# Performance work log

Measured on AMD Instinct MI355X. Metric: run time of the kernel, lower is better.

Reference implementation:

```python
import jax, jax.numpy as jnp
import numpy as np

TIME_STEP = 0.1
ITER_NUM = 10
ALPHA = 0.01


def _conv3x3(x, w, b):
    # x: [N,C,H,W], w: [O,C,3,3], b: [O]; SAME padding, stride 1
    y = jax.lax.conv_general_dilated(
        x, w, window_strides=(1, 1), padding=((1, 1), (1, 1)),
        dimension_numbers=("NCHW", "OIHW", "NCHW"))
    return y + b[None, :, None, None]


def _nonlin(x, alpha=ALPHA):
    y = jnp.minimum(x, 1.0 + alpha * (x - 1.0))
    return jnp.maximum(y, -1.0 + alpha * (y + 1.0))


def setup_inputs() -> dict:
    key = jax.random.key(0)
    ks = jax.random.split(key, 8)
    N, Ci, Co, H, W = 16, 64, 64, 128, 128
    fan_in = Ci * 9
    bound = 1.0 / np.sqrt(fan_in)
    x = jax.random.normal(ks[0], (N, Ci, H, W), dtype=jnp.float32)
    rescale_w = jax.random.uniform(ks[1], (Co, Ci, 3, 3), minval=-bound, maxval=bound, dtype=jnp.float32)
    rescale_b = jax.random.uniform(ks[2], (Co,), minval=-bound, maxval=bound, dtype=jnp.float32)
    bound_a = 1.0 / np.sqrt(Co * 9)
    A_w = jax.random.uniform(ks[3], (Co, Co, 3, 3), minval=-bound_a, maxval=bound_a, dtype=jnp.float32)
    A_b = jax.random.uniform(ks[4], (Co,), minval=-bound_a, maxval=bound_a, dtype=jnp.float32)
    B_w = jax.random.uniform(ks[5], (Co, Ci, 3, 3), minval=-bound, maxval=bound, dtype=jnp.float32)
    B_b = jax.random.uniform(ks[6], (Co,), minval=-bound, maxval=bound, dtype=jnp.float32)
    Z = jax.random.normal(ks[7], (Co,), dtype=jnp.float32)
    return {"x": x, "rescale_w": rescale_w, "rescale_b": rescale_b,
            "A_w": A_w, "A_b": A_b, "B_w": B_w, "B_b": B_b, "Z": Z}


def reference(x, rescale_w, rescale_b, A_w, A_b, B_w, B_b, Z):
    input_coupling = _conv3x3(x, B_w, B_b) + Z[None, :, None, None]
    state = _conv3x3(x, rescale_w, rescale_b)

    def body(i, s):
        coupling = _conv3x3(_nonlin(s), A_w, A_b) + input_coupling
        return s + TIME_STEP * (-s + coupling)

    state = jax.lax.fori_loop(0, ITER_NUM, body, state)
    return _nonlin(state)
```

## Files before the change

kernel.cpp:

```cpp
#include <hip/hip_runtime.h>


typedef short  bf16x8 __attribute__((ext_vector_type(8)));
typedef float  f32x4  __attribute__((ext_vector_type(4)));

#define HH 128
#define WW 128
#define NCH 64
#define GROWS 8
#define NSLOT 10
#define XS 32
#define NC 34
#define ROWB 128
#define SLOTB (NC * ROWB)
#define ACTB (NSLOT * SLOTB)
#define WSETB 73728

__device__ __align__(16) unsigned char g_fw[3 * WSETB];

__device__ __forceinline__ float nonlin(float x) {
    const float A = 0.01f;
    float y = fminf(x, fmaf(A, x, 1.0f - A));
    return fmaxf(y, fmaf(A, y, -(1.0f - A)));
}
__device__ __forceinline__ unsigned int f2bf(float f) {
    unsigned int u = __float_as_uint(f);
    u += 0x7fffu + ((u >> 16) & 1u);
    return u >> 16;
}

__global__ __launch_bounds__(256)
void prep_w(const float* __restrict__ rw, const float* __restrict__ bw,
            const float* __restrict__ aw) {
    const float* w = blockIdx.x == 0 ? rw : (blockIdx.x == 1 ? bw : aw);
    unsigned char* o = g_fw + blockIdx.x * WSETB;
    int chunk = blockIdx.y * 256 + threadIdx.x;
    int cb  = chunk / 1152;
    int rem = chunk - cb * 1152;
    int kb  = rem >> 6;
    int ln  = rem & 63;
    int cout = cb * 16 + (ln & 15);
    int g    = ln >> 4;
    unsigned int h[8];
    #pragma unroll
    for (int j = 0; j < 8; ++j) {
        int k = kb * 32 + g * 8 + j;
        int tap = k >> 6;
        int cin = k & 63;
        h[j] = f2bf(w[(cout * 64 + cin) * 9 + tap]);
    }
    uint4 v;
    v.x = h[0] | (h[1] << 16);
    v.y = h[2] | (h[3] << 16);
    v.z = h[4] | (h[5] << 16);
    v.w = h[6] | (h[7] << 16);
    *(uint4*)(o + chunk * 16) = v;
}

__device__ __forceinline__ void conv_tile(const char* actl, const unsigned char* fw,
                                          int lane, int wv, f32x4 (&acc)[4][4]) {
    const int l15 = lane & 15;
    const int g4  = lane >> 4;
    #pragma unroll
    for (int kb = 0; kb < 18; ++kb) {
        const int tap  = kb >> 1;
        const int dy   = tap / 3;
        const int dx   = tap - dy * 3;
        const int cinB = (kb & 1) * 64 + g4 * 16;
        bf16x8 af[4];
        #pragma unroll
        for (int cb = 0; cb < 4; ++cb)
            af[cb] = *(const bf16x8*)(fw + ((cb * 18 + kb) * 64 + lane) * 16);
        bf16x8 bfr[4];
        #pragma unroll
        for (int i = 0; i < 4; ++i) {
            int row = wv * 2 + (i >> 1) + dy;
            int c   = (i & 1) * 16 + l15 + dx;
            bfr[i] = *(const bf16x8*)(actl + row * SLOTB + c * ROWB
                                      + (cinB ^ ((c & 7) << 4)));
        }
        #pragma unroll
        for (int cb = 0; cb < 4; ++cb)
            #pragma unroll
            for (int i = 0; i < 4; ++i)
                acc[cb][i] = __builtin_amdgcn_mfma_f32_16x16x32_bf16(
                    af[cb], bfr[i], acc[cb][i], 0, 0, 0);
    }
}

template<int MODE>
__global__ __launch_bounds__(256, 3)
void cenn(const float* __restrict__ src,
          const float* __restrict__ rb, const float* __restrict__ bb,
          const float* __restrict__ zz, const float* __restrict__ ab,
          const float* __restrict__ icp,
          float* __restrict__ dst, float* __restrict__ dst2)
{
    __shared__ __align__(16) char actl[ACTB];
    const int tid  = threadIdx.x;
    const int lane = tid & 63;
    const int wv   = tid >> 6;
    const int l15  = lane & 15;
    const int g4   = lane >> 4;

    int lin = (blockIdx.z * 16 + blockIdx.y) * 4 + blockIdx.x;
    lin = (lin & 7) * 128 + (lin >> 3);
    const int x0 = (lin & 3) * XS;
    const int y0 = ((lin >> 2) & 15) * GROWS;
    const int n  = lin >> 6;

    if constexpr (MODE == 0) {
        for (int idx = tid; idx < NSLOT * NC * 8; idx += 256) {
            int r   = idx / (NC * 8);
            int rem = idx - r * (NC * 8);
            int cb8 = rem / NC;
            int c   = rem - cb8 * NC;
            int y   = y0 + r - 1;
            int x   = x0 + c - 1;
            uint4 v = {0u, 0u, 0u, 0u};
            if ((unsigned)y < (unsigned)HH && (unsigned)x < (unsigned)WW) {
                const float* p = src + ((size_t)(n * NCH + cb8 * 8) * HH + y) * WW + x;
                unsigned int h[8];
                #pragma unroll
                for (int j = 0; j < 8; ++j)
                    h[j] = f2bf(p[(size_t)j * HH * WW]);
                v.x = h[0] | (h[1] << 16);
                v.y = h[2] | (h[3] << 16);
                v.z = h[4] | (h[5] << 16);
                v.w = h[6] | (h[7] << 16);
            }
            *(uint4*)(actl + r * SLOTB + c * ROWB + ((cb8 * 16) ^ ((c & 7) << 4))) = v;
        }
    } else {
        for (int idx = tid; idx < NSLOT * NC * 16; idx += 256) {
            int r   = idx / (NC * 16);
            int rem = idx - r * (NC * 16);
            int c   = rem >> 4;
            int q   = rem & 15;
            int y   = y0 + r - 1;
            int x   = x0 + c - 1;
            uint2 w2 = {0u, 0u};
            if ((unsigned)y < (unsigned)HH && (unsigned)x < (unsigned)WW) {
                f32x4 v = *(const f32x4*)(src + ((((size_t)n * HH + y) * WW + x) << 6) + q * 4);
                w2.x = f2bf(nonlin(v[0])) | (f2bf(nonlin(v[1])) << 16);
                w2.y = f2bf(nonlin(v[2])) | (f2bf(nonlin(v[3])) << 16);
            }
            *(uint2*)(actl + r * SLOTB + c * ROWB + ((q * 8) ^ ((c & 7) << 4))) = w2;
        }
    }
    __syncthreads();

    f32x4 acc[4][4];
    #pragma unroll
    for (int a = 0; a < 4; ++a)
        #pragma unroll
        for (int b = 0; b < 4; ++b)
            acc[a][b] = (f32x4){0.f, 0.f, 0.f, 0.f};

    conv_tile(actl, g_fw + (MODE == 0 ? 0 : 2 * WSETB), lane, wv, acc);

    if constexpr (MODE == 0) {
        #pragma unroll
        for (int cb = 0; cb < 4; ++cb)
            #pragma unroll
            for (int i = 0; i < 4; ++i) {
                int y  = y0 + wv * 2 + (i >> 1);
                int x  = x0 + (i & 1) * 16 + l15;
                int c0 = cb * 16 + g4 * 4;
                size_t base = ((((size_t)n * HH + y) * WW + x) << 6) + c0;
                f32x4 o;
                #pragma unroll
                for (int r = 0; r < 4; ++r) o[r] = acc[cb][i][r] + rb[c0 + r];
                *(f32x4*)(dst + base) = o;
            }
        #pragma unroll
        for (int a = 0; a < 4; ++a)
            #pragma unroll
            for (int b = 0; b < 4; ++b)
                acc[a][b] = (f32x4){0.f, 0.f, 0.f, 0.f};
        conv_tile(actl, g_fw + WSETB, lane, wv, acc);
        #pragma unroll
        for (int cb = 0; cb < 4; ++cb)
            #pragma unroll
            for (int i = 0; i < 4; ++i) {
                int y  = y0 + wv * 2 + (i >> 1);
                int x  = x0 + (i & 1) * 16 + l15;
                int c0 = cb * 16 + g4 * 4;
                size_t base = ((((size_t)n * HH + y) * WW + x) << 6) + c0;
                f32x4 o;
                #pragma unroll
                for (int r = 0; r < 4; ++r)
                    o[r] = 0.1f * (acc[cb][i][r] + bb[c0 + r] + zz[c0 + r] + ab[c0 + r]);
                *(f32x4*)(dst2 + base) = o;
            }
    } else {
        #pragma unroll
        for (int rs = 0; rs < 2; ++rs) {
            __syncthreads();
            #pragma unroll
            for (int cb = 0; cb < 4; ++cb)
                #pragma unroll
                for (int fr = 0; fr < 2; ++fr) {
                    int i  = rs * 2 + fr;
                    int x  = fr * 16 + l15;
                    int cs = (cb * 16 + g4 * 4) ^ ((x & 7) << 2);
                    *(f32x4*)(actl + (((wv * 32 + x) << 6) + cs) * 4) = acc[cb][i];
                }
            __syncthreads();
            #pragma unroll
            for (int ps = 0; ps < 8; ++ps) {
                int t2   = ps * 256 + tid;
                int q    = t2 & 15;
                int px   = t2 >> 4;
                int x    = px & 31;
                int lrow = px >> 5;
                int cs   = (q * 4) ^ ((x & 7) << 2);
                f32x4 cv = *(const f32x4*)(actl + (((lrow * 32 + x) << 6) + cs) * 4);
                int y  = y0 + lrow * 2 + rs;
                int gx = x0 + x;
                size_t base = ((((size_t)n * HH + y) * WW + gx) << 6) + q * 4;
                f32x4 s = *(const f32x4*)(src + base);
                f32x4 p = *(const f32x4*)(icp + base);
                f32x4 o;
                #pragma unroll
                for (int r = 0; r < 4; ++r)
                    o[r] = 0.1f * cv[r] + 0.9f * s[r] + p[r];
                if constexpr (MODE == 1) {
                    *(f32x4*)(dst + base) = o;
                } else {
                    #pragma unroll
                    for (int r = 0; r < 4; ++r) o[r] = nonlin(o[r]);
                    *(f32x4*)(actl + (((lrow * 32 + x) << 6) + cs) * 4) = o;
                }
            }
            if constexpr (MODE == 2) {
                __syncthreads();
                #pragma unroll
                for (int ps = 0; ps < 8; ++ps) {
                    int xl   = tid & 15;
                    int xf   = (tid >> 4) & 1;
                    int qh   = tid >> 5;
                    int q    = (ps & 1) * 8 + qh;
                    int lrow = ps >> 1;
                    int x    = xf * 16 + xl;
                    int cs   = (q * 4) ^ ((x & 7) << 2);
                    f32x4 v  = *(const f32x4*)(actl + (((lrow * 32 + x) << 6) + cs) * 4);
                    int y  = y0 + lrow * 2 + rs;
                    int gx = x0 + x;
                    #pragma unroll
                    for (int j = 0; j < 4; ++j)
                        dst[((size_t)(n * NCH + q * 4 + j) * HH + y) * WW + gx] = v[j];
                }
            }
        }
    }
}

extern "C" void kernel_launch(void* const* d_in, const int* in_sizes, int n_in,
                              void* d_out, int out_size, void* d_ws, size_t ws_size,
                              hipStream_t stream) {
    const float* x  = (const float*)d_in[0];
    const float* rw = (const float*)d_in[1];
    const float* rb = (const float*)d_in[2];
    const float* aw = (const float*)d_in[3];
    const float* ab = (const float*)d_in[4];
    const float* bw = (const float*)d_in[5];
    const float* bb = (const float*)d_in[6];
    const float* z  = (const float*)d_in[7];
    float* out = (float*)d_out;

    const size_t P = (size_t)16 * NCH * HH * WW;
    float* icp = (float*)d_ws;
    float* s1  = icp + P;

    dim3 blk(256, 1, 1), grd(4, 16, 16);

    prep_w<<<dim3(3, 18, 1), blk, 0, stream>>>(rw, bw, aw);
    cenn<0><<<grd, blk, 0, stream>>>(x, rb, bb, z, ab, nullptr, out, icp);

    for (int i = 0; i < 10; ++i) {
        const float* s = (i & 1) ? s1 : out;
        float*       d = (i & 1) ? out : s1;
        if (i == 9)
            cenn<2><<<grd, blk, 0, stream>>>(s, nullptr, nullptr, nullptr, nullptr, icp, out, nullptr);
        else
            cenn<1><<<grd, blk, 0, stream>>>(s, nullptr, nullptr, nullptr, nullptr, icp, d, nullptr);
    }
}
```

Before: 619.9 us.

## Store input coupling in bf16 and fuse init convolutions into one pass

The precomputed input-coupling tensor is now stored as bf16 instead of fp32, which halves that read in each of the ten iteration kernels. The init kernel runs both convolutions in one interleaved MFMA loop sharing the activation fragments, using two accumulator sets and lowering the occupancy hint to 2. Init outputs are now written through an LDS transpose for coalesced stores. The cost is extra rounding error in the coupling term and higher register pressure in the init kernel.

```diff
diff --git a/kernel.cpp b/kernel.cpp
--- a/kernel.cpp
+++ b/kernel.cpp
@@ -88,13 +88,50 @@
     }
 }
 
-template<int MODE>
-__global__ __launch_bounds__(256, 3)
-void cenn(const float* __restrict__ src,
-          const float* __restrict__ rb, const float* __restrict__ bb,
-          const float* __restrict__ zz, const float* __restrict__ ab,
-          const float* __restrict__ icp,
-          float* __restrict__ dst, float* __restrict__ dst2)
+__device__ __forceinline__ void conv_tile2(const char* actl,
+                                           const unsigned char* fw0,
+                                           const unsigned char* fw1,
+                                           int lane, int wv,
+                                           f32x4 (&acc0)[4][4], f32x4 (&acc1)[4][4]) {
+    const int l15 = lane & 15;
+    const int g4  = lane >> 4;
+    #pragma unroll
+    for (int kb = 0; kb < 18; ++kb) {
+        const int tap  = kb >> 1;
+        const int dy   = tap / 3;
+        const int dx   = tap - dy * 3;
+        const int cinB = (kb & 1) * 64 + g4 * 16;
+        bf16x8 af0[4], af1[4];
+        #pragma unroll
+        for (int cb = 0; cb < 4; ++cb) {
+            af0[cb] = *(const bf16x8*)(fw0 + ((cb * 18 + kb) * 64 + lane) * 16);
+            af1[cb] = *(const bf16x8*)(fw1 + ((cb * 18 + kb) * 64 + lane) * 16);
+        }
+        bf16x8 bfr[4];
+        #pragma unroll
+        for (int i = 0; i < 4; ++i) {
+            int row = wv * 2 + (i >> 1) + dy;
+            int c   = (i & 1) * 16 + l15 + dx;
+            bfr[i] = *(const bf16x8*)(actl + row * SLOTB + c * ROWB
+                                      + (cinB ^ ((c & 7) << 4)));
+        }
+        #pragma unroll
+        for (int cb = 0; cb < 4; ++cb)
+            #pragma unroll
+            for (int i = 0; i < 4; ++i) {
+                acc0[cb][i] = __builtin_amdgcn_mfma_f32_16x16x32_bf16(
+                    af0[cb], bfr[i], acc0[cb][i], 0, 0, 0);
+                acc1[cb][i] = __builtin_amdgcn_mfma_f32_16x16x32_bf16(
+                    af1[cb], bfr[i], acc1[cb][i], 0, 0, 0);
+            }
+    }
+}
+
+__global__ __launch_bounds__(256, 2)
+void cenn_init(const float* __restrict__ src,
+               const float* __restrict__ rb, const float* __restrict__ bb,
+               const float* __restrict__ zz, const float* __restrict__ ab,
+               float* __restrict__ dst, unsigned short* __restrict__ icp)
 {
     __shared__ __align__(16) char actl[ACTB];
     const int tid  = threadIdx.x;
@@ -109,44 +146,143 @@
     const int y0 = ((lin >> 2) & 15) * GROWS;
     const int n  = lin >> 6;
 
-    if constexpr (MODE == 0) {
-        for (int idx = tid; idx < NSLOT * NC * 8; idx += 256) {
-            int r   = idx / (NC * 8);
-            int rem = idx - r * (NC * 8);
-            int cb8 = rem / NC;
-            int c   = rem - cb8 * NC;
-            int y   = y0 + r - 1;
-            int x   = x0 + c - 1;
-            uint4 v = {0u, 0u, 0u, 0u};
-            if ((unsigned)y < (unsigned)HH && (unsigned)x < (unsigned)WW) {
-                const float* p = src + ((size_t)(n * NCH + cb8 * 8) * HH + y) * WW + x;
-                unsigned int h[8];
-                #pragma unroll
-                for (int j = 0; j < 8; ++j)
-                    h[j] = f2bf(p[(size_t)j * HH * WW]);
-                v.x = h[0] | (h[1] << 16);
-                v.y = h[2] | (h[3] << 16);
-                v.z = h[4] | (h[5] << 16);
-                v.w = h[6] | (h[7] << 16);
-            }
-            *(uint4*)(actl + r * SLOTB + c * ROWB + ((cb8 * 16) ^ ((c & 7) << 4))) = v;
-        }
-    } else {
-        for (int idx = tid; idx < NSLOT * NC * 16; idx += 256) {
-            int r   = idx / (NC * 16);
-            int rem = idx - r * (NC * 16);
-            int c   = rem >> 4;
-            int q   = rem & 15;
-            int y   = y0 + r - 1;
-            int x   = x0 + c - 1;
-            uint2 w2 = {0u, 0u};
-            if ((unsigned)y < (unsigned)HH && (unsigned)x < (unsigned)WW) {
-                f32x4 v = *(const f32x4*)(src + ((((size_t)n * HH + y) * WW + x) << 6) + q * 4);
-                w2.x = f2bf(nonlin(v[0])) | (f2bf(nonlin(v[1])) << 16);
-                w2.y = f2bf(nonlin(v[2])) | (f2bf(nonlin(v[3])) << 16);
-            }
-            *(uint2*)(actl + r * SLOTB + c * ROWB + ((q * 8) ^ ((c & 7) << 4))) = w2;
-        }
+    for (int idx = tid; idx < NSLOT * NC * 8; idx += 256) {
+        int r   = idx / (NC * 8);
+        int rem = idx - r * (NC * 8);
+        int cb8 = rem / NC;
+        int c   = rem - cb8 * NC;
+        int y   = y0 + r - 1;
+        int x   = x0 + c - 1;
+        uint4 v = {0u, 0u, 0u, 0u};
+        if ((unsigned)y < (unsigned)HH && (unsigned)x < (unsigned)WW) {
+            const float* p = src + ((size_t)(n * NCH + cb8 * 8) * HH + y) * WW + x;
+            unsigned int h[8];
+            #pragma unroll
+            for (int j = 0; j < 8; ++j)
+                h[j] = f2bf(p[(size_t)j * HH * WW]);
+            v.x = h[0] | (h[1] << 16);
+            v.y = h[2] | (h[3] << 16);
+            v.z = h[4] | (h[5] << 16);
+            v.w = h[6] | (h[7] << 16);
+        }
+        *(uint4*)(actl + r * SLOTB + c * ROWB + ((cb8 * 16) ^ ((c & 7) << 4))) = v;
+    }
+    __syncthreads();
+
+    f32x4 acc0[4][4], acc1[4][4];
+    #pragma unroll
+    for (int a = 0; a < 4; ++a)
+        #pragma unroll
+        for (int b = 0; b < 4; ++b) {
+            acc0[a][b] = (f32x4){0.f, 0.f, 0.f, 0.f};
+            acc1[a][b] = (f32x4){0.f, 0.f, 0.f, 0.f};
+        }
+    conv_tile2(actl, g_fw, g_fw + WSETB, lane, wv, acc0, acc1);
+
+    const int q = tid & 15;
+    f32x4 brb = *(const f32x4*)(rb + q * 4);
+    f32x4 bic;
+    {
+        f32x4 b1 = *(const f32x4*)(bb + q * 4);
+        f32x4 b2 = *(const f32x4*)(zz + q * 4);
+        f32x4 b3 = *(const f32x4*)(ab + q * 4);
+        #pragma unroll
+        for (int r = 0; r < 4; ++r) bic[r] = 0.1f * (b1[r] + b2[r] + b3[r]);
+    }
+
+    #pragma unroll
+    for (int rs = 0; rs < 2; ++rs) {
+        __syncthreads();
+        #pragma unroll
+        for (int cb = 0; cb < 4; ++cb)
+            #pragma unroll
+            for (int fr = 0; fr < 2; ++fr) {
+                int x  = fr * 16 + l15;
+                int cs = (cb * 16 + g4 * 4) ^ ((x & 7) << 2);
+                *(f32x4*)(actl + (((wv * 32 + x) << 6) + cs) * 4) = acc0[cb][rs * 2 + fr];
+            }
+        __syncthreads();
+        #pragma unroll
+        for (int ps = 0; ps < 8; ++ps) {
+            int t2   = ps * 256 + tid;
+            int px   = t2 >> 4;
+            int x    = px & 31;
+            int lrow = px >> 5;
+            int cs   = (q * 4) ^ ((x & 7) << 2);
+            f32x4 cv = *(const f32x4*)(actl + (((lrow * 32 + x) << 6) + cs) * 4);
+            int y  = y0 + lrow * 2 + rs;
+            int gx = x0 + x;
+            size_t base = ((((size_t)n * HH + y) * WW + gx) << 6) + q * 4;
+            f32x4 o;
+            #pragma unroll
+            for (int r = 0; r < 4; ++r) o[r] = cv[r] + brb[r];
+            *(f32x4*)(dst + base) = o;
+        }
+        __syncthreads();
+        #pragma unroll
+        for (int cb = 0; cb < 4; ++cb)
+            #pragma unroll
+            for (int fr = 0; fr < 2; ++fr) {
+                int x  = fr * 16 + l15;
+                int cs = (cb * 16 + g4 * 4) ^ ((x & 7) << 2);
+                *(f32x4*)(actl + (((wv * 32 + x) << 6) + cs) * 4) = acc1[cb][rs * 2 + fr];
+            }
+        __syncthreads();
+        #pragma unroll
+        for (int ps = 0; ps < 8; ++ps) {
+            int t2   = ps * 256 + tid;
+            int px   = t2 >> 4;
+            int x    = px & 31;
+            int lrow = px >> 5;
+            int cs   = (q * 4) ^ ((x & 7) << 2);
+            f32x4 cv = *(const f32x4*)(actl + (((lrow * 32 + x) << 6) + cs) * 4);
+            int y  = y0 + lrow * 2 + rs;
+            int gx = x0 + x;
+            size_t base = ((((size_t)n * HH + y) * WW + gx) << 6) + q * 4;
+            f32x4 o;
+            #pragma unroll
+            for (int r = 0; r < 4; ++r) o[r] = 0.1f * cv[r] + bic[r];
+            uint2 w2;
+            w2.x = f2bf(o[0]) | (f2bf(o[1]) << 16);
+            w2.y = f2bf(o[2]) | (f2bf(o[3]) << 16);
+            *(uint2*)(icp + base) = w2;
+        }
+    }
+}
+
+template<int FINAL>
+__global__ __launch_bounds__(256, 3)
+void cenn_iter(const float* __restrict__ src,
+               const unsigned short* __restrict__ icp,
+               float* __restrict__ dst)
+{
+    __shared__ __align__(16) char actl[ACTB];
+    const int tid  = threadIdx.x;
+    const int lane = tid & 63;
+    const int wv   = tid >> 6;
+    const int l15  = lane & 15;
+    const int g4   = lane >> 4;
+
+    int lin = (blockIdx.z * 16 + blockIdx.y) * 4 + blockIdx.x;
+    lin = (lin & 7) * 128 + (lin >> 3);
+    const int x0 = (lin & 3) * XS;
+    const int y0 = ((lin >> 2) & 15) * GROWS;
+    const int n  = lin >> 6;
+
+    for (int idx = tid; idx < NSLOT * NC * 16; idx += 256) {
+        int r   = idx / (NC * 16);
+        int rem = idx - r * (NC * 16);
+        int c   = rem >> 4;
+        int qq  = rem & 15;
+        int y   = y0 + r - 1;
+        int x   = x0 + c - 1;
+        uint2 w2 = {0u, 0u};
+        if ((unsigned)y < (unsigned)HH && (unsigned)x < (unsigned)WW) {
+            f32x4 v = *(const f32x4*)(src + ((((size_t)n * HH + y) * WW + x) << 6) + qq * 4);
+            w2.x = f2bf(nonlin(v[0])) | (f2bf(nonlin(v[1])) << 16);
+            w2.y = f2bf(nonlin(v[2])) | (f2bf(nonlin(v[3])) << 16);
+        }
+        *(uint2*)(actl + r * SLOTB + c * ROWB + ((qq * 8) ^ ((c & 7) << 4))) = w2;
     }
     __syncthreads();
 
@@ -157,100 +293,68 @@
         for (int b = 0; b < 4; ++b)
             acc[a][b] = (f32x4){0.f, 0.f, 0.f, 0.f};
 
-    conv_tile(actl, g_fw + (MODE == 0 ? 0 : 2 * WSETB), lane, wv, acc);
-
-    if constexpr (MODE == 0) {
-        #pragma unroll
-        for (int cb = 0; cb < 4; ++cb)
-            #pragma unroll
-            for (int i = 0; i < 4; ++i) {
-                int y  = y0 + wv * 2 + (i >> 1);
-                int x  = x0 + (i & 1) * 16 + l15;
-                int c0 = cb * 16 + g4 * 4;
-                size_t base = ((((size_t)n * HH + y) * WW + x) << 6) + c0;
-                f32x4 o;
+    conv_tile(actl, g_fw + 2 * WSETB, lane, wv, acc);
+
+    const int q = tid & 15;
+    #pragma unroll
+    for (int rs = 0; rs < 2; ++rs) {
+        __syncthreads();
+        #pragma unroll
+        for (int cb = 0; cb < 4; ++cb)
+            #pragma unroll
+            for (int fr = 0; fr < 2; ++fr) {
+                int x  = fr * 16 + l15;
+                int cs = (cb * 16 + g4 * 4) ^ ((x & 7) << 2);
+                *(f32x4*)(actl + (((wv * 32 + x) << 6) + cs) * 4) = acc[cb][rs * 2 + fr];
+            }
+        __syncthreads();
+        #pragma unroll
+        for (int ps = 0; ps < 8; ++ps) {
+            int t2   = ps * 256 + tid;
+            int px   = t2 >> 4;
+            int x    = px & 31;
+            int lrow = px >> 5;
+            int cs   = (q * 4) ^ ((x & 7) << 2);
+            f32x4 cv = *(const f32x4*)(actl + (((lrow * 32 + x) << 6) + cs) * 4);
+            int y  = y0 + lrow * 2 + rs;
+            int gx = x0 + x;
+            size_t base = ((((size_t)n * HH + y) * WW + gx) << 6) + q * 4;
+            f32x4 s = *(const f32x4*)(src + base);
+            uint2 pw = *(const uint2*)(icp + base);
+            f32x4 p;
+            p[0] = __uint_as_float(pw.x << 16);
+            p[1] = __uint_as_float(pw.x & 0xffff0000u);
+            p[2] = __uint_as_float(pw.y << 16);
+            p[3] = __uint_as_float(pw.y & 0xffff0000u);
+            f32x4 o;
+            #pragma unroll
+            for (int r = 0; r < 4; ++r)
+                o[r] = 0.1f * cv[r] + 0.9f * s[r] + p[r];
+            if constexpr (FINAL == 0) {
+                *(f32x4*)(dst + base) = o;
+            } else {
                 #pragma unroll
-                for (int r = 0; r < 4; ++r) o[r] = acc[cb][i][r] + rb[c0 + r];
-                *(f32x4*)(dst + base) = o;
-            }
-        #pragma unroll
-        for (int a = 0; a < 4; ++a)
-            #pragma unroll
-            for (int b = 0; b < 4; ++b)
-                acc[a][b] = (f32x4){0.f, 0.f, 0.f, 0.f};
-        conv_tile(actl, g_fw + WSETB, lane, wv, acc);
-        #pragma unroll
-        for (int cb = 0; cb < 4; ++cb)
-            #pragma unroll
-            for (int i = 0; i < 4; ++i) {
-                int y  = y0 + wv * 2 + (i >> 1);
-                int x  = x0 + (i & 1) * 16 + l15;
-                int c0 = cb * 16 + g4 * 4;
-                size_t base = ((((size_t)n * HH + y) * WW + x) << 6) + c0;
-                f32x4 o;
-                #pragma unroll
-                for (int r = 0; r < 4; ++r)
-                    o[r] = 0.1f * (acc[cb][i][r] + bb[c0 + r] + zz[c0 + r] + ab[c0 + r]);
-                *(f32x4*)(dst2 + base) = o;
-            }
-    } else {
-        #pragma unroll
-        for (int rs = 0; rs < 2; ++rs) {
+                for (int r = 0; r < 4; ++r) o[r] = nonlin(o[r]);
+                *(f32x4*)(actl + (((lrow * 32 + x) << 6) + cs) * 4) = o;
+            }
+        }
+        if constexpr (FINAL == 1) {
             __syncthreads();
             #pragma unroll
-            for (int cb = 0; cb < 4; ++cb)
-                #pragma unroll
-                for (int fr = 0; fr < 2; ++fr) {
-                    int i  = rs * 2 + fr;
-                    int x  = fr * 16 + l15;
-                    int cs = (cb * 16 + g4 * 4) ^ ((x & 7) << 2);
-                    *(f32x4*)(actl + (((wv * 32 + x) << 6) + cs) * 4) = acc[cb][i];
-                }
-            __syncthreads();
-            #pragma unroll
             for (int ps = 0; ps < 8; ++ps) {
-                int t2   = ps * 256 + tid;
-                int q    = t2 & 15;
-                int px   = t2 >> 4;
-                int x    = px & 31;
-                int lrow = px >> 5;
-                int cs   = (q * 4) ^ ((x & 7) << 2);
-                f32x4 cv = *(const f32x4*)(actl + (((lrow * 32 + x) << 6) + cs) * 4);
+                int xl   = tid & 15;
+                int xf   = (tid >> 4) & 1;
+                int qh   = tid >> 5;
+                int qc   = (ps & 1) * 8 + qh;
+                int lrow = ps >> 1;
+                int x    = xf * 16 + xl;
+                int cs   = (qc * 4) ^ ((x & 7) << 2);
+                f32x4 v  = *(const f32x4*)(actl + (((lrow * 32 + x) << 6) + cs) * 4);
                 int y  = y0 + lrow * 2 + rs;
                 int gx = x0 + x;
-                size_t base = ((((size_t)n * HH + y) * WW + gx) << 6) + q * 4;
-                f32x4 s = *(const f32x4*)(src + base);
-                f32x4 p = *(const f32x4*)(icp + base);
-                f32x4 o;
                 #pragma unroll
-                for (int r = 0; r < 4; ++r)
-                    o[r] = 0.1f * cv[r] + 0.9f * s[r] + p[r];
-                if constexpr (MODE == 1) {
-                    *(f32x4*)(dst + base) = o;
-                } else {
-                    #pragma unroll
-                    for (int r = 0; r < 4; ++r) o[r] = nonlin(o[r]);
-                    *(f32x4*)(actl + (((lrow * 32 + x) << 6) + cs) * 4) = o;
-                }
-            }
-            if constexpr (MODE == 2) {
-                __syncthreads();
-                #pragma unroll
-                for (int ps = 0; ps < 8; ++ps) {
-                    int xl   = tid & 15;
-                    int xf   = (tid >> 4) & 1;
-                    int qh   = tid >> 5;
-                    int q    = (ps & 1) * 8 + qh;
-                    int lrow = ps >> 1;
-                    int x    = xf * 16 + xl;
-                    int cs   = (q * 4) ^ ((x & 7) << 2);
-                    f32x4 v  = *(const f32x4*)(actl + (((lrow * 32 + x) << 6) + cs) * 4);
-                    int y  = y0 + lrow * 2 + rs;
-                    int gx = x0 + x;
-                    #pragma unroll
-                    for (int j = 0; j < 4; ++j)
-                        dst[((size_t)(n * NCH + q * 4 + j) * HH + y) * WW + gx] = v[j];
-                }
+                for (int j = 0; j < 4; ++j)
+                    dst[((size_t)(n * NCH + qc * 4 + j) * HH + y) * WW + gx] = v[j];
             }
         }
     }
@@ -270,20 +374,20 @@
     float* out = (float*)d_out;
 
     const size_t P = (size_t)16 * NCH * HH * WW;
-    float* icp = (float*)d_ws;
-    float* s1  = icp + P;
+    unsigned short* icp = (unsigned short*)d_ws;
+    float* s1 = (float*)((char*)d_ws + 2 * P);
 
     dim3 blk(256, 1, 1), grd(4, 16, 16);
 
     prep_w<<<dim3(3, 18, 1), blk, 0, stream>>>(rw, bw, aw);
-    cenn<0><<<grd, blk, 0, stream>>>(x, rb, bb, z, ab, nullptr, out, icp);
+    cenn_init<<<grd, blk, 0, stream>>>(x, rb, bb, z, ab, out, icp);
 
     for (int i = 0; i < 10; ++i) {
         const float* s = (i & 1) ? s1 : out;
         float*       d = (i & 1) ? out : s1;
         if (i == 9)
-            cenn<2><<<grd, blk, 0, stream>>>(s, nullptr, nullptr, nullptr, nullptr, icp, out, nullptr);
+            cenn_iter<1><<<grd, blk, 0, stream>>>(s, icp, out);
         else
-            cenn<1><<<grd, blk, 0, stream>>>(s, nullptr, nullptr, nullptr, nullptr, icp, d, nullptr);
-    }
-}
+            cenn_iter<0><<<grd, blk, 0, stream>>>(s, icp, d);
+    }
+}
```

Result: no change. 621.3 us (+0.2%).

## Store input coupling in bf16 and reuse interior state loads in registers

Applied to the files above, without the earlier changes.

The precomputed input-coupling term is now stored as bf16 instead of fp32, which halves its read traffic in each of the ten iteration kernels. The iteration kernel also loads the halo cells separately from the interior. Interior state values are read once, converted to bf16 activations in shared memory, and the first row-half is kept in registers for the state update instead of being re-read from global memory. The cost is lower precision in the coupling term, which is added to the state every iteration.

```diff
diff --git a/kernel.cpp b/kernel.cpp
--- a/kernel.cpp
+++ b/kernel.cpp
@@ -88,13 +88,11 @@
     }
 }
 
-template<int MODE>
 __global__ __launch_bounds__(256, 3)
-void cenn(const float* __restrict__ src,
-          const float* __restrict__ rb, const float* __restrict__ bb,
-          const float* __restrict__ zz, const float* __restrict__ ab,
-          const float* __restrict__ icp,
-          float* __restrict__ dst, float* __restrict__ dst2)
+void cenn_init(const float* __restrict__ src,
+               const float* __restrict__ rb, const float* __restrict__ bb,
+               const float* __restrict__ zz, const float* __restrict__ ab,
+               float* __restrict__ dst, unsigned short* __restrict__ icp)
 {
     __shared__ __align__(16) char actl[ACTB];
     const int tid  = threadIdx.x;
@@ -109,36 +107,108 @@
     const int y0 = ((lin >> 2) & 15) * GROWS;
     const int n  = lin >> 6;
 
-    if constexpr (MODE == 0) {
-        for (int idx = tid; idx < NSLOT * NC * 8; idx += 256) {
-            int r   = idx / (NC * 8);
-            int rem = idx - r * (NC * 8);
-            int cb8 = rem / NC;
-            int c   = rem - cb8 * NC;
-            int y   = y0 + r - 1;
-            int x   = x0 + c - 1;
-            uint4 v = {0u, 0u, 0u, 0u};
-            if ((unsigned)y < (unsigned)HH && (unsigned)x < (unsigned)WW) {
-                const float* p = src + ((size_t)(n * NCH + cb8 * 8) * HH + y) * WW + x;
-                unsigned int h[8];
-                #pragma unroll
-                for (int j = 0; j < 8; ++j)
-                    h[j] = f2bf(p[(size_t)j * HH * WW]);
-                v.x = h[0] | (h[1] << 16);
-                v.y = h[2] | (h[3] << 16);
-                v.z = h[4] | (h[5] << 16);
-                v.w = h[6] | (h[7] << 16);
-            }
-            *(uint4*)(actl + r * SLOTB + c * ROWB + ((cb8 * 16) ^ ((c & 7) << 4))) = v;
-        }
-    } else {
-        for (int idx = tid; idx < NSLOT * NC * 16; idx += 256) {
-            int r   = idx / (NC * 16);
-            int rem = idx - r * (NC * 16);
-            int c   = rem >> 4;
-            int q   = rem & 15;
-            int y   = y0 + r - 1;
-            int x   = x0 + c - 1;
+    for (int idx = tid; idx < NSLOT * NC * 8; idx += 256) {
+        int r   = idx / (NC * 8);
+        int rem = idx - r * (NC * 8);
+        int cb8 = rem / NC;
+        int c   = rem - cb8 * NC;
+        int y   = y0 + r - 1;
+        int x   = x0 + c - 1;
+        uint4 v = {0u, 0u, 0u, 0u};
+        if ((unsigned)y < (unsigned)HH && (unsigned)x < (unsigned)WW) {
+            const float* p = src + ((size_t)(n * NCH + cb8 * 8) * HH + y) * WW + x;
+            unsigned int h[8];
+            #pragma unroll
+            for (int j = 0; j < 8; ++j)
+                h[j] = f2bf(p[(size_t)j * HH * WW]);
+            v.x = h[0] | (h[1] << 16);
+            v.y = h[2] | (h[3] << 16);
+            v.z = h[4] | (h[5] << 16);
+            v.w = h[6] | (h[7] << 16);
+        }
+        *(uint4*)(actl + r * SLOTB + c * ROWB + ((cb8 * 16) ^ ((c & 7) << 4))) = v;
+    }
+    __syncthreads();
+
+    f32x4 acc[4][4];
+    #pragma unroll
+    for (int a = 0; a < 4; ++a)
+        #pragma unroll
+        for (int b = 0; b < 4; ++b)
+            acc[a][b] = (f32x4){0.f, 0.f, 0.f, 0.f};
+
+    conv_tile(actl, g_fw, lane, wv, acc);
+    #pragma unroll
+    for (int cb = 0; cb < 4; ++cb)
+        #pragma unroll
+        for (int i = 0; i < 4; ++i) {
+            int y  = y0 + wv * 2 + (i >> 1);
+            int x  = x0 + (i & 1) * 16 + l15;
+            int c0 = cb * 16 + g4 * 4;
+            size_t base = ((((size_t)n * HH + y) * WW + x) << 6) + c0;
+            f32x4 o;
+            #pragma unroll
+            for (int r = 0; r < 4; ++r) o[r] = acc[cb][i][r] + rb[c0 + r];
+            *(f32x4*)(dst + base) = o;
+        }
+
+    #pragma unroll
+    for (int a = 0; a < 4; ++a)
+        #pragma unroll
+        for (int b = 0; b < 4; ++b)
+            acc[a][b] = (f32x4){0.f, 0.f, 0.f, 0.f};
+    conv_tile(actl, g_fw + WSETB, lane, wv, acc);
+    #pragma unroll
+    for (int cb = 0; cb < 4; ++cb)
+        #pragma unroll
+        for (int i = 0; i < 4; ++i) {
+            int y  = y0 + wv * 2 + (i >> 1);
+            int x  = x0 + (i & 1) * 16 + l15;
+            int c0 = cb * 16 + g4 * 4;
+            size_t base = ((((size_t)n * HH + y) * WW + x) << 6) + c0;
+            f32x4 o;
+            #pragma unroll
+            for (int r = 0; r < 4; ++r)
+                o[r] = 0.1f * (acc[cb][i][r] + bb[c0 + r] + zz[c0 + r] + ab[c0 + r]);
+            uint2 w2;
+            w2.x = f2bf(o[0]) | (f2bf(o[1]) << 16);
+            w2.y = f2bf(o[2]) | (f2bf(o[3]) << 16);
+            *(uint2*)(icp + base) = w2;
+        }
+}
+
+template<int FINAL>
+__global__ __launch_bounds__(256, 3)
+void cenn_iter(const float* __restrict__ src,
+               const unsigned short* __restrict__ icp,
+               float* __restrict__ dst)
+{
+    __shared__ __align__(16) char actl[ACTB];
+    const int tid  = threadIdx.x;
+    const int lane = tid & 63;
+    const int wv   = tid >> 6;
+    const int l15  = lane & 15;
+    const int g4   = lane >> 4;
+
+    int lin = (blockIdx.z * 16 + blockIdx.y) * 4 + blockIdx.x;
+    lin = (lin & 7) * 128 + (lin >> 3);
+    const int x0 = (lin & 3) * XS;
+    const int y0 = ((lin >> 2) & 15) * GROWS;
+    const int n  = lin >> 6;
+
+    const int qq = tid & 15;
+
+    #pragma unroll
+    for (int j = 0; j < 6; ++j) {
+        int idx = j * 256 + tid;
+        if (idx < 1344) {
+            int cell = idx >> 4;
+            int q    = idx & 15;
+            int r, c;
+            if (cell < 68) { r = (cell < 34) ? 0 : 9; c = (cell < 34) ? cell : cell - 34; }
+            else           { int e = cell - 68; r = 1 + (e >> 1); c = (e & 1) ? 33 : 0; }
+            int y = y0 + r - 1;
+            int x = x0 + c - 1;
             uint2 w2 = {0u, 0u};
             if ((unsigned)y < (unsigned)HH && (unsigned)x < (unsigned)WW) {
                 f32x4 v = *(const f32x4*)(src + ((((size_t)n * HH + y) * WW + x) << 6) + q * 4);
@@ -148,6 +218,27 @@
             *(uint2*)(actl + r * SLOTB + c * ROWB + ((q * 8) ^ ((c & 7) << 4))) = w2;
         }
     }
+
+    f32x4 sreg[8];
+    #pragma unroll
+    for (int rs = 0; rs < 2; ++rs)
+        #pragma unroll
+        for (int ps = 0; ps < 8; ++ps) {
+            int t2   = ps * 256 + tid;
+            int px   = t2 >> 4;
+            int x    = px & 31;
+            int lrow = px >> 5;
+            int y    = y0 + lrow * 2 + rs;
+            int gx   = x0 + x;
+            f32x4 v  = *(const f32x4*)(src + ((((size_t)n * HH + y) * WW + gx) << 6) + qq * 4);
+            if (rs == 0) sreg[ps] = v;
+            int r = lrow * 2 + rs + 1;
+            int c = x + 1;
+            uint2 w2;
+            w2.x = f2bf(nonlin(v[0])) | (f2bf(nonlin(v[1])) << 16);
+            w2.y = f2bf(nonlin(v[2])) | (f2bf(nonlin(v[3])) << 16);
+            *(uint2*)(actl + r * SLOTB + c * ROWB + ((qq * 8) ^ ((c & 7) << 4))) = w2;
+        }
     __syncthreads();
 
     f32x4 acc[4][4];
@@ -157,100 +248,69 @@
         for (int b = 0; b < 4; ++b)
             acc[a][b] = (f32x4){0.f, 0.f, 0.f, 0.f};
 
-    conv_tile(actl, g_fw + (MODE == 0 ? 0 : 2 * WSETB), lane, wv, acc);
-
-    if constexpr (MODE == 0) {
+    conv_tile(actl, g_fw + 2 * WSETB, lane, wv, acc);
+
+    #pragma unroll
+    for (int rs = 0; rs < 2; ++rs) {
+        __syncthreads();
         #pragma unroll
         for (int cb = 0; cb < 4; ++cb)
             #pragma unroll
-            for (int i = 0; i < 4; ++i) {
-                int y  = y0 + wv * 2 + (i >> 1);
-                int x  = x0 + (i & 1) * 16 + l15;
-                int c0 = cb * 16 + g4 * 4;
-                size_t base = ((((size_t)n * HH + y) * WW + x) << 6) + c0;
-                f32x4 o;
+            for (int fr = 0; fr < 2; ++fr) {
+                int x  = fr * 16 + l15;
+                int cs = (cb * 16 + g4 * 4) ^ ((x & 7) << 2);
+                *(f32x4*)(actl + (((wv * 32 + x) << 6) + cs) * 4) = acc[cb][rs * 2 + fr];
+            }
+        __syncthreads();
+        #pragma unroll
+        for (int ps = 0; ps < 8; ++ps) {
+            int t2   = ps * 256 + tid;
+            int px   = t2 >> 4;
+            int x    = px & 31;
+            int lrow = px >> 5;
+            int cs   = (qq * 4) ^ ((x & 7) << 2);
+            f32x4 cv = *(const f32x4*)(actl + (((lrow * 32 + x) << 6) + cs) * 4);
+            int y  = y0 + lrow * 2 + rs;
+            int gx = x0 + x;
+            size_t base = ((((size_t)n * HH + y) * WW + gx) << 6) + qq * 4;
+            f32x4 s;
+            if (rs == 0) s = sreg[ps];
+            else         s = *(const f32x4*)(src + base);
+            uint2 pw = *(const uint2*)(icp + base);
+            f32x4 p;
+            p[0] = __uint_as_float(pw.x << 16);
+            p[1] = __uint_as_float(pw.x & 0xffff0000u);
+            p[2] = __uint_as_float(pw.y << 16);
+            p[3] = __uint_as_float(pw.y & 0xffff0000u);
+            f32x4 o;
+            #pragma unroll
+            for (int r = 0; r < 4; ++r)
+                o[r] = 0.1f * cv[r] + 0.9f * s[r] + p[r];
+            if constexpr (FINAL == 0) {
+                *(f32x4*)(dst + base) = o;
+            } else {
                 #pragma unroll
-                for (int r = 0; r < 4; ++r) o[r] = acc[cb][i][r] + rb[c0 + r];
-                *(f32x4*)(dst + base) = o;
+                for (int r = 0; r < 4; ++r) o[r] = nonlin(o[r]);
+                *(f32x4*)(actl + (((lrow * 32 + x) << 6) + cs) * 4) = o;
             }
-        #pragma unroll
-        for (int a = 0; a < 4; ++a)
-            #pragma unroll
-            for (int b = 0; b < 4; ++b)
-                acc[a][b] = (f32x4){0.f, 0.f, 0.f, 0.f};
-        conv_tile(actl, g_fw + WSETB, lane, wv, acc);
-        #pragma unroll
-        for (int cb = 0; cb < 4; ++cb)
-            #pragma unroll
-            for (int i = 0; i < 4; ++i) {
-                int y  = y0 + wv * 2 + (i >> 1);
-                int x  = x0 + (i & 1) * 16 + l15;
-                int c0 = cb * 16 + g4 * 4;
-                size_t base = ((((size_t)n * HH + y) * WW + x) << 6) + c0;
-                f32x4 o;
-                #pragma unroll
-                for (int r = 0; r < 4; ++r)
-                    o[r] = 0.1f * (acc[cb][i][r] + bb[c0 + r] + zz[c0 + r] + ab[c0 + r]);
-                *(f32x4*)(dst2 + base) = o;
-            }
-    } else {
-        #pragma unroll
-        for (int rs = 0; rs < 2; ++rs) {
+        }
+        if constexpr (FINAL == 1) {
             __syncthreads();
             #pragma unroll
-            for (int cb = 0; cb < 4; ++cb)
-                #pragma unroll
-                for (int fr = 0; fr < 2; ++fr) {
-                    int i  = rs * 2 + fr;
-                    int x  = fr * 16 + l15;
-                    int cs = (cb * 16 + g4 * 4) ^ ((x & 7) << 2);
-                    *(f32x4*)(actl + (((wv * 32 + x) << 6) + cs) * 4) = acc[cb][i];
-                }
-            __syncthreads();
-            #pragma unroll
             for (int ps = 0; ps < 8; ++ps) {
-                int t2   = ps * 256 + tid;
-                int q    = t2 & 15;
-                int px   = t2 >> 4;
-                int x    = px & 31;
-                int lrow = px >> 5;
-                int cs   = (q * 4) ^ ((x & 7) << 2);
-                f32x4 cv = *(const f32x4*)(actl + (((lrow * 32 + x) << 6) + cs) * 4);
+                int xl   = tid & 15;
+                int xf   = (tid >> 4) & 1;
+                int qh   = tid >> 5;
+                int qc   = (ps & 1) * 8 + qh;
+                int lrow = ps >> 1;
+                int x    = xf * 16 + xl;
+                int cs   = (qc * 4) ^ ((x & 7) << 2);
+                f32x4 v  = *(const f32x4*)(actl + (((lrow * 32 + x) << 6) + cs) * 4);
                 int y  = y0 + lrow * 2 + rs;
                 int gx = x0 + x;
-                size_t base = ((((size_t)n * HH + y) * WW + gx) << 6) + q * 4;
-                f32x4 s = *(const f32x4*)(src + base);
-                f32x4 p = *(const f32x4*)(icp + base);
-                f32x4 o;
                 #pragma unroll
-                for (int r = 0; r < 4; ++r)
-                    o[r] = 0.1f * cv[r] + 0.9f * s[r] + p[r];
-                if constexpr (MODE == 1) {
-                    *(f32x4*)(dst + base) = o;
-                } else {
-                    #pragma unroll
-                    for (int r = 0; r < 4; ++r) o[r] = nonlin(o[r]);
-                    *(f32x4*)(actl + (((lrow * 32 + x) << 6) + cs) * 4) = o;
-                }
-            }
-            if constexpr (MODE == 2) {
-                __syncthreads();
-                #pragma unroll
-                for (int ps = 0; ps < 8; ++ps) {
-                    int xl   = tid & 15;
-                    int xf   = (tid >> 4) & 1;
-                    int qh   = tid >> 5;
-                    int q    = (ps & 1) * 8 + qh;
-                    int lrow = ps >> 1;
-                    int x    = xf * 16 + xl;
-                    int cs   = (q * 4) ^ ((x & 7) << 2);
-                    f32x4 v  = *(const f32x4*)(actl + (((lrow * 32 + x) << 6) + cs) * 4);
-                    int y  = y0 + lrow * 2 + rs;
-                    int gx = x0 + x;
-                    #pragma unroll
-                    for (int j = 0; j < 4; ++j)
-                        dst[((size_t)(n * NCH + q * 4 + j) * HH + y) * WW + gx] = v[j];
-                }
+                for (int j = 0; j < 4; ++j)
+                    dst[((size_t)(n * NCH + qc * 4 + j) * HH + y) * WW + gx] = v[j];
             }
         }
     }
@@ -270,20 +330,20 @@
     float* out = (float*)d_out;
 
     const size_t P = (size_t)16 * NCH * HH * WW;
-    float* icp = (float*)d_ws;
-    float* s1  = icp + P;
+    unsigned short* icp = (unsigned short*)d_ws;
+    float* s1 = (float*)((char*)d_ws + 2 * P);
 
     dim3 blk(256, 1, 1), grd(4, 16, 16);
 
     prep_w<<<dim3(3, 18, 1), blk, 0, stream>>>(rw, bw, aw);
-    cenn<0><<<grd, blk, 0, stream>>>(x, rb, bb, z, ab, nullptr, out, icp);
+    cenn_init<<<grd, blk, 0, stream>>>(x, rb, bb, z, ab, out, icp);
 
     for (int i = 0; i < 10; ++i) {
         const float* s = (i & 1) ? s1 : out;
         float*       d = (i & 1) ? out : s1;
         if (i == 9)
-            cenn<2><<<grd, blk, 0, stream>>>(s, nullptr, nullptr, nullptr, nullptr, icp, out, nullptr);
+            cenn_iter<1><<<grd, blk, 0, stream>>>(s, icp, out);
         else
-            cenn<1><<<grd, blk, 0, stream>>>(s, nullptr, nullptr, nullptr, nullptr, icp, d, nullptr);
-    }
-}
+            cenn_iter<0><<<grd, blk, 0, stream>>>(s, icp, d);
+    }
+}
```

New measurement: 788.5 us. +27.2%, slower.
